# Kernel optimization log

Measured on AMD Instinct MI355X. Metric: run time of the kernel, lower is better.

The kernel has to match this reference:

```python
import jax, jax.numpy as jnp
import numpy as np

B, D, H, DOUT, E, K = 8192, 1024, 4096, 1024, 8, 2


def setup_inputs() -> dict:
    key = jax.random.key(0)
    ks = jax.random.split(key, 7)
    s_d = 1.0 / np.sqrt(D)
    s_h = 1.0 / np.sqrt(H)
    return {
        "x": jax.random.normal(ks[0], (B, D), jnp.float32),
        "Wg": jax.random.uniform(ks[1], (D, E), jnp.float32, -s_d, s_d),
        "bg": jax.random.uniform(ks[2], (E,), jnp.float32, -s_d, s_d),
        "W1": jax.random.uniform(ks[3], (E, D, H), jnp.float32, -s_d, s_d),
        "b1": jax.random.uniform(ks[4], (E, H), jnp.float32, -s_d, s_d),
        "W2": jax.random.uniform(ks[5], (E, H, DOUT), jnp.float32, -s_h, s_h),
        "b2": jax.random.uniform(ks[6], (E, DOUT), jnp.float32, -s_h, s_h),
    }


def reference(x, Wg, bg, W1, b1, W2, b2):
    # gating
    gate_probs = jax.nn.softmax(x @ Wg + bg, axis=-1)          # [B, E]
    top_k_probs, top_k_idx = jax.lax.top_k(gate_probs, K)       # [B, K]
    top_k_probs = top_k_probs / jnp.sum(top_k_probs, axis=-1, keepdims=True)

    # dense all-expert compute (faithful to torch.stack over experts)
    h = jax.nn.gelu(jnp.einsum('bd,edh->beh', x, W1) + b1, approximate=False)  # [B, E, H]
    expert_outputs = jnp.einsum('beh,eho->beo', h, W2) + b2                    # [B, E, DOUT]

    # gather selected experts and combine
    sel = jnp.take_along_axis(expert_outputs, top_k_idx[:, :, None], axis=1)   # [B, K, DOUT]
    output = jnp.sum(sel * top_k_probs[:, :, None], axis=1)                    # [B, DOUT]

    # load-balancing aux loss (as written in the original)
    expert_usage = jnp.mean(gate_probs, axis=0)                # [E]
    uniform = jnp.full_like(expert_usage, 1.0 / E)
    aux_loss = jnp.sum(expert_usage * jnp.log(uniform) - jnp.log(expert_usage) * uniform)
    return output, aux_loss
```

## Files before the change

kernel.cpp:

```cpp
#include <hip/hip_runtime.h>
#include <hip/hip_bf16.h>
#include <hip/hip_fp16.h>

#define B_    8192
#define D_    1024
#define H_    4096
#define DOUT_ 1024
#define E_    8
#define MAXR  17408

typedef float    f32x4 __attribute__((ext_vector_type(4)));
typedef _Float16 f16x8 __attribute__((ext_vector_type(8)));
typedef unsigned short u16;
typedef u16      u16x8 __attribute__((ext_vector_type(8)));
typedef u16      u16x4 __attribute__((ext_vector_type(4)));
typedef unsigned int u32;

__device__ __forceinline__ u16 f2h_bits(float f) {
  _Float16 h = (_Float16)f;
  return __builtin_bit_cast(u16, h);
}
__device__ __forceinline__ float h2f(u16 b) {
  return (float)__builtin_bit_cast(_Float16, b);
}

__device__ __forceinline__ float gelu_f(float v) {
  float z = 0.7978845608028654f * (v + 0.044715f * v * v * v);
  float ez = __expf(2.f * z);
  float th = 1.f - 2.f / (ez + 1.f);
  return 0.5f * v * (1.f + th);
}

#define OFF_TOPI 512
#define OFF_TOPW (OFF_TOPI + 65536)
#define OFF_ATOK (OFF_TOPW + 65536)
#define OFF_WSL  (OFF_ATOK + 69632)
#define OFF_SLOT (OFF_WSL + 69632)
#define OFF_XG   524288
#define OFF_W1T  (OFF_XG + 35651584)
#define OFF_W2T  OFF_XG
#define OFF_Y    (OFF_XG + 67108864)
#define OFF_HB   (OFF_W1T + 67108864)

__global__ void k_init(int* __restrict__ atok, float* __restrict__ wslot,
                       int* __restrict__ meta) {
  int i = blockIdx.x * 256 + threadIdx.x;
  if (i < MAXR) { atok[i] = 0; wslot[i] = 0.f; }
  if (blockIdx.x == 0 && threadIdx.x < 64) meta[threadIdx.x] = 0;
}

__global__ __launch_bounds__(256) void k_gate(
    const float* __restrict__ x, const float* __restrict__ Wg,
    const float* __restrict__ bg, int* __restrict__ counts,
    float* __restrict__ usage, int* __restrict__ topi, float* __restrict__ topw) {
  __shared__ float su[E_];
  if (threadIdx.x < E_) su[threadIdx.x] = 0.f;
  __syncthreads();
  const int lane = threadIdx.x & 63;
  const int b = blockIdx.x * 4 + (threadIdx.x >> 6);
  float p[E_] = {0.f,0.f,0.f,0.f,0.f,0.f,0.f,0.f};
  #pragma unroll
  for (int j = 0; j < 4; ++j) {
    int d = j * 256 + lane * 4;
    float4 xv = *(const float4*)&x[(size_t)b * D_ + d];
    const float* wr = &Wg[(size_t)d * E_];
    #pragma unroll
    for (int c = 0; c < 4; ++c) {
      float xc = reinterpret_cast<const float*>(&xv)[c];
      #pragma unroll
      for (int e = 0; e < E_; ++e) p[e] += xc * wr[c * E_ + e];
    }
  }
  #pragma unroll
  for (int off = 32; off >= 1; off >>= 1)
    #pragma unroll
    for (int e = 0; e < E_; ++e) p[e] += __shfl_xor(p[e], off, 64);
  float mx = -1e30f;
  #pragma unroll
  for (int e = 0; e < E_; ++e) { p[e] += bg[e]; mx = fmaxf(mx, p[e]); }
  int i0 = 0; float l0 = p[0];
  #pragma unroll
  for (int e = 1; e < E_; ++e) if (p[e] > l0) { l0 = p[e]; i0 = e; }
  int i1 = -1; float l1 = -1e30f;
  #pragma unroll
  for (int e = 0; e < E_; ++e) if (e != i0 && p[e] > l1) { l1 = p[e]; i1 = e; }
  float s = 0.f;
  #pragma unroll
  for (int e = 0; e < E_; ++e) { p[e] = expf(p[e] - mx); s += p[e]; }
  float inv = 1.f / s;
  if (lane == 0) {
    float e0 = expf(l0 - mx), e1 = expf(l1 - mx);
    float wsum = e0 + e1;
    topi[b * 2] = i0; topi[b * 2 + 1] = i1;
    topw[b * 2] = e0 / wsum; topw[b * 2 + 1] = e1 / wsum;
    atomicAdd(&counts[i0], 1);
    atomicAdd(&counts[i1], 1);
    #pragma unroll
    for (int e = 0; e < E_; ++e) atomicAdd(&su[e], p[e] * inv);
  }
  __syncthreads();
  if (threadIdx.x < E_) atomicAdd(&usage[threadIdx.x], su[threadIdx.x]);
}

__global__ void k_scan_aux(const int* __restrict__ counts, int* __restrict__ offsets,
                           const float* __restrict__ usage, float* __restrict__ auxp) {
  if (threadIdx.x == 0) {
    int off = 0;
    for (int e = 0; e < E_; ++e) { offsets[e] = off; off += (counts[e] + 127) & ~127; }
    offsets[E_] = off;
    float aux = 0.f;
    const float lu = logf(1.0f / (float)E_);
    for (int e = 0; e < E_; ++e) {
      float u = usage[e] * (1.0f / (float)B_);
      aux += u * lu - logf(u) * (1.0f / (float)E_);
    }
    *auxp = aux;
  }
}

__global__ void k_scatter(const int* __restrict__ topi, const float* __restrict__ topw,
                          const int* __restrict__ offsets, int* __restrict__ cursors,
                          int* __restrict__ atok, float* __restrict__ wslot,
                          int* __restrict__ slot_of) {
  int b = blockIdx.x * 256 + threadIdx.x;
  if (b >= B_) return;
  #pragma unroll
  for (int k = 0; k < 2; ++k) {
    int e = topi[b * 2 + k];
    int pos = atomicAdd(&cursors[e], 1);
    int slot = offsets[e] + pos;
    atok[slot] = b;
    wslot[slot] = topw[b * 2 + k];
    slot_of[b * 2 + k] = slot;
  }
}

__global__ __launch_bounds__(256) void k_gather(const float* __restrict__ x,
                                                const int* __restrict__ atok,
                                                u16* __restrict__ Xg) {
  int slot = blockIdx.x;
  int tok = atok[slot];
  int c = threadIdx.x * 4;
  float4 v = *(const float4*)&x[(size_t)tok * D_ + c];
  const float* vf = reinterpret_cast<const float*>(&v);
  u16x4 o;
  o.x = f2h_bits(vf[0]); o.y = f2h_bits(vf[1]);
  o.z = f2h_bits(vf[2]); o.w = f2h_bits(vf[3]);
  *(u16x4*)&Xg[(size_t)slot * D_ + c] = o;
}

__global__ __launch_bounds__(256) void k_cvt_t(const float* __restrict__ src,
                                               u16* __restrict__ dst, int K, int N) {
  const int e = blockIdx.z;
  const int kt = blockIdx.x * 64;
  const int nt = blockIdx.y * 64;
  __shared__ u16 t[64][68];
  const float* s = src + (size_t)e * K * N;
  u16* d = dst + (size_t)e * N * K;
  const int tr = threadIdx.x >> 4;
  const int tc = threadIdx.x & 15;
  #pragma unroll
  for (int i = 0; i < 4; ++i) {
    int k = tr + i * 16;
    float4 v = *(const float4*)&s[(size_t)(kt + k) * N + nt + tc * 4];
    t[k][tc*4+0] = f2h_bits(v.x); t[k][tc*4+1] = f2h_bits(v.y);
    t[k][tc*4+2] = f2h_bits(v.z); t[k][tc*4+3] = f2h_bits(v.w);
  }
  __syncthreads();
  #pragma unroll
  for (int i = 0; i < 4; ++i) {
    int n = tr + i * 16;
    u16x4 o;
    o.x = t[tc*4+0][n]; o.y = t[tc*4+1][n];
    o.z = t[tc*4+2][n]; o.w = t[tc*4+3][n];
    *(u16x4*)&d[(size_t)(nt + n) * K + kt + tc * 4] = o;
  }
}

#define GLDS(g, l) __builtin_amdgcn_global_load_lds( \
    (const u32 __attribute__((address_space(1)))*)(g), \
    (u32 __attribute__((address_space(3)))*)(l), 16, 0, 0)

#define VMWAIT(N) asm volatile("s_waitcnt vmcnt(" #N ")" ::: "memory")
#define BARRIER() do { __builtin_amdgcn_s_barrier(); \
                       asm volatile("" ::: "memory"); } while (0)

#define NXT(x) ((x) == 24576 ? 0 : (x) + 12288)

#define STG3(LDK, kt, sb) do { \
  const int r_ = lane >> 2; \
  const int sc_ = ((lane & 3) ^ ((r_ ^ (r_ >> 2)) & 3)) * 8; \
  { \
    int rw = wid * 16 + r_; \
    GLDS(Ap + (size_t)rw * (LDK) + (kt) * 32 + sc_, SM + (sb) + wid * 512); \
  } \
  _Pragma("unroll") \
  for (int j = 0; j < 2; ++j) { \
    int seg = wid * 2 + j; \
    GLDS(Bp + (size_t)(seg * 16 + r_) * (LDK) + (kt) * 32 + sc_, \
         SM + (sb) + 4096 + seg * 512); \
  } } while (0)

#define RD_FR(rb_) do { \
  const int r15_ = lane & 15; \
  const int co_ = (((lane >> 4) ^ ((r15_ ^ (r15_ >> 2)) & 3)) * 8); \
  _Pragma("unroll") \
  for (int mi = 0; mi < 4; ++mi) \
    af[mi] = *(const f16x8*)&SM[(rb_) + (wr * 64 + mi * 16 + r15_) * 32 + co_]; \
  _Pragma("unroll") \
  for (int n = 0; n < 4; ++n) \
    bf[n] = *(const f16x8*)&SM[(rb_) + 4096 + (wc * 64 + n * 16 + r15_) * 32 + co_]; \
} while (0)

#define MM16() do { \
  __builtin_amdgcn_s_setprio(1); \
  _Pragma("unroll") \
  for (int mi = 0; mi < 4; ++mi) \
    _Pragma("unroll") \
    for (int n = 0; n < 4; ++n) \
      acc[mi][n] = __builtin_amdgcn_mfma_f32_16x16x32_f16(af[mi], bf[n], acc[mi][n], 0, 0, 0); \
  __builtin_amdgcn_s_setprio(0); \
} while (0)

#define KLOOP(LDK, NT) do { \
  int rb = 0, wb = 24576; \
  STG3(LDK, 0, 0); \
  STG3(LDK, 1, 12288); \
  VMWAIT(3); \
  BARRIER(); \
  for (int t = 0; t < (NT); ++t) { \
    RD_FR(rb); \
    if (t + 2 < (NT)) STG3(LDK, t + 2, wb); \
    BARRIER(); \
    MM16(); \
    if (t + 2 < (NT)) VMWAIT(3); \
    else if (t + 1 < (NT)) VMWAIT(0); \
    BARRIER(); \
    rb = NXT(rb); wb = NXT(wb); \
  } \
} while (0)

__global__ __launch_bounds__(512, 4) void k_gemm1(
    const u16* __restrict__ Xg, const u16* __restrict__ W1t,
    const float* __restrict__ b1, const int* __restrict__ offsets,
    u16* __restrict__ Hb) {
  const int L = blockIdx.x;
  const int mtile = L >> 4;
  const int nt = L & 15;
  const int row0 = mtile * 128;
  if (row0 >= offsets[E_]) return;
  int e = 0;
  #pragma unroll
  for (int i = 1; i < E_; ++i) e = (row0 >= offsets[i]) ? i : e;
  const int n0 = nt * 256;
  const int tid = threadIdx.x, lane = tid & 63, wid = tid >> 6;
  const int wr = wid >> 2, wc = wid & 3;
  __shared__ __align__(16) u16 SM[36864];
  f32x4 acc[4][4] = {};
  f16x8 af[4], bf[4];
  const u16* Ap = Xg + (size_t)row0 * D_;
  const u16* Bp = W1t + (size_t)e * H_ * D_ + (size_t)n0 * D_;

  KLOOP(D_, 32);

  const int rhi = (lane >> 4) * 4, cix = lane & 15;
  float bv[4];
  #pragma unroll
  for (int n = 0; n < 4; ++n) bv[n] = b1[e * H_ + n0 + wc * 64 + n * 16 + cix];
  #pragma unroll
  for (int r = 0; r < 2; ++r) {
    if (wr == r) {
      #pragma unroll
      for (int m = 0; m < 4; ++m)
        #pragma unroll
        for (int n = 0; n < 4; ++n)
          #pragma unroll
          for (int j = 0; j < 4; ++j)
            SM[(m * 16 + rhi + j) * 264 + wc * 64 + n * 16 + cix] =
                f2h_bits(gelu_f(acc[m][n][j] + bv[n]));
    }
    __syncthreads();
    {
      const int rl = tid >> 3, co = (tid & 7) * 32;
      u16* dst = &Hb[(size_t)(row0 + r * 64 + rl) * H_ + n0 + co];
      const u16* srcp = &SM[rl * 264 + co];
      #pragma unroll
      for (int qq = 0; qq < 4; ++qq)
        *(u16x8*)(dst + qq * 8) = *(const u16x8*)(srcp + qq * 8);
    }
    __syncthreads();
  }
}

__global__ __launch_bounds__(512, 4) void k_gemm2(
    const u16* __restrict__ Hb, const u16* __restrict__ W2t,
    const float* __restrict__ b2, const int* __restrict__ offsets,
    u16* __restrict__ Y) {
  const int L = blockIdx.x;
  const int mtile = L >> 2;
  const int nt = L & 3;
  const int row0 = mtile * 128;
  if (row0 >= offsets[E_]) return;
  int e = 0;
  #pragma unroll
  for (int i = 1; i < E_; ++i) e = (row0 >= offsets[i]) ? i : e;
  const int n0 = nt * 256;
  const int tid = threadIdx.x, lane = tid & 63, wid = tid >> 6;
  const int wr = wid >> 2, wc = wid & 3;
  __shared__ __align__(16) u16 SM[36864];
  f32x4 acc[4][4] = {};
  f16x8 af[4], bf[4];
  const u16* Ap = Hb + (size_t)row0 * H_;
  const u16* Bp = W2t + (size_t)e * DOUT_ * H_ + (size_t)n0 * H_;

  KLOOP(H_, 128);

  const int rhi = (lane >> 4) * 4, cix = lane & 15;
  float bv[4];
  #pragma unroll
  for (int n = 0; n < 4; ++n) bv[n] = b2[e * DOUT_ + n0 + wc * 64 + n * 16 + cix];
  #pragma unroll
  for (int r = 0; r < 2; ++r) {
    if (wr == r) {
      #pragma unroll
      for (int m = 0; m < 4; ++m)
        #pragma unroll
        for (int n = 0; n < 4; ++n)
          #pragma unroll
          for (int j = 0; j < 4; ++j)
            SM[(m * 16 + rhi + j) * 264 + wc * 64 + n * 16 + cix] =
                f2h_bits(acc[m][n][j] + bv[n]);
    }
    __syncthreads();
    {
      const int rl = tid >> 3, co = (tid & 7) * 32;
      u16* dst = &Y[(size_t)(row0 + r * 64 + rl) * DOUT_ + n0 + co];
      const u16* srcp = &SM[rl * 264 + co];
      #pragma unroll
      for (int qq = 0; qq < 4; ++qq)
        *(u16x8*)(dst + qq * 8) = *(const u16x8*)(srcp + qq * 8);
    }
    __syncthreads();
  }
}

__global__ __launch_bounds__(256) void k_combine(
    const u16* __restrict__ Y, const float* __restrict__ topw,
    const int* __restrict__ slot_of, float* __restrict__ out) {
  const int b = blockIdx.x;
  const int c = threadIdx.x * 4;
  const int s0 = slot_of[b * 2], s1 = slot_of[b * 2 + 1];
  const float w0 = topw[b * 2], w1 = topw[b * 2 + 1];
  u16x4 y0 = *(const u16x4*)&Y[(size_t)s0 * DOUT_ + c];
  u16x4 y1 = *(const u16x4*)&Y[(size_t)s1 * DOUT_ + c];
  float4 o;
  o.x = w0 * h2f(y0.x) + w1 * h2f(y1.x);
  o.y = w0 * h2f(y0.y) + w1 * h2f(y1.y);
  o.z = w0 * h2f(y0.z) + w1 * h2f(y1.z);
  o.w = w0 * h2f(y0.w) + w1 * h2f(y1.w);
  *(float4*)&out[(size_t)b * DOUT_ + c] = o;
}

extern "C" void kernel_launch(void* const* d_in, const int* in_sizes, int n_in,
                              void* d_out, int out_size, void* d_ws, size_t ws_size,
                              hipStream_t stream) {
  const float* x  = (const float*)d_in[0];
  const float* Wg = (const float*)d_in[1];
  const float* bg = (const float*)d_in[2];
  const float* W1 = (const float*)d_in[3];
  const float* b1 = (const float*)d_in[4];
  const float* W2 = (const float*)d_in[5];
  const float* b2 = (const float*)d_in[6];
  float* out = (float*)d_out;

  char* ws = (char*)d_ws;
  int*   counts  = (int*)(ws + 0);
  int*   cursors = (int*)(ws + 32);
  int*   offsets = (int*)(ws + 64);
  float* usage   = (float*)(ws + 128);
  int*   topi    = (int*)(ws + OFF_TOPI);
  float* topw    = (float*)(ws + OFF_TOPW);
  int*   atok    = (int*)(ws + OFF_ATOK);
  float* wslot   = (float*)(ws + OFF_WSL);
  int*   slot_of = (int*)(ws + OFF_SLOT);
  u16*   Xg      = (u16*)(ws + OFF_XG);
  u16*   W1t     = (u16*)(ws + OFF_W1T);
  u16*   W2t     = (u16*)(ws + OFF_W2T);
  u16*   Y       = (u16*)(ws + OFF_Y);
  u16*   Hb      = (u16*)(ws + OFF_HB);

  k_init<<<(MAXR + 255) / 256, 256, 0, stream>>>(atok, wslot, (int*)ws);
  k_gate<<<B_ / 4, 256, 0, stream>>>(x, Wg, bg, counts, usage, topi, topw);
  k_scan_aux<<<1, 64, 0, stream>>>(counts, offsets, usage, out + (size_t)B_ * DOUT_);
  k_scatter<<<B_ / 256, 256, 0, stream>>>(topi, topw, offsets, cursors, atok, wslot, slot_of);
  k_gather<<<MAXR, 256, 0, stream>>>(x, atok, Xg);
  k_cvt_t<<<dim3(D_ / 64, H_ / 64, E_), 256, 0, stream>>>(W1, W1t, D_, H_);
  k_gemm1<<<(MAXR / 128) * 16, 512, 0, stream>>>(Xg, W1t, b1, offsets, Hb);
  k_cvt_t<<<dim3(H_ / 64, DOUT_ / 64, E_), 256, 0, stream>>>(W2, W2t, H_, DOUT_);
  k_gemm2<<<(MAXR / 128) * 4, 512, 0, stream>>>(Hb, W2t, b2, offsets, Y);
  k_combine<<<B_, 256, 0, stream>>>(Y, topw, slot_of, out);
}
```

Baseline: 800.6 us.

## Remap GEMM tiles per XCD, widen transpose stores, drop unused slot weights

```diff
diff --git a/kernel.cpp b/kernel.cpp
--- a/kernel.cpp
+++ b/kernel.cpp
@@ -34,18 +34,16 @@
 #define OFF_TOPI 512
 #define OFF_TOPW (OFF_TOPI + 65536)
 #define OFF_ATOK (OFF_TOPW + 65536)
-#define OFF_WSL  (OFF_ATOK + 69632)
-#define OFF_SLOT (OFF_WSL + 69632)
+#define OFF_SLOT (OFF_ATOK + 69632)
 #define OFF_XG   524288
 #define OFF_W1T  (OFF_XG + 35651584)
 #define OFF_W2T  OFF_XG
 #define OFF_Y    (OFF_XG + 67108864)
 #define OFF_HB   (OFF_W1T + 67108864)
 
-__global__ void k_init(int* __restrict__ atok, float* __restrict__ wslot,
-                       int* __restrict__ meta) {
+__global__ void k_init(int* __restrict__ atok, int* __restrict__ meta) {
   int i = blockIdx.x * 256 + threadIdx.x;
-  if (i < MAXR) { atok[i] = 0; wslot[i] = 0.f; }
+  if (i < MAXR) atok[i] = 0;
   if (blockIdx.x == 0 && threadIdx.x < 64) meta[threadIdx.x] = 0;
 }
 
@@ -118,9 +116,8 @@
   }
 }
 
-__global__ void k_scatter(const int* __restrict__ topi, const float* __restrict__ topw,
-                          const int* __restrict__ offsets, int* __restrict__ cursors,
-                          int* __restrict__ atok, float* __restrict__ wslot,
+__global__ void k_scatter(const int* __restrict__ topi, const int* __restrict__ offsets,
+                          int* __restrict__ cursors, int* __restrict__ atok,
                           int* __restrict__ slot_of) {
   int b = blockIdx.x * 256 + threadIdx.x;
   if (b >= B_) return;
@@ -130,7 +127,6 @@
     int pos = atomicAdd(&cursors[e], 1);
     int slot = offsets[e] + pos;
     atok[slot] = b;
-    wslot[slot] = topw[b * 2 + k];
     slot_of[b * 2 + k] = slot;
   }
 }
@@ -154,27 +150,26 @@
   const int e = blockIdx.z;
   const int kt = blockIdx.x * 64;
   const int nt = blockIdx.y * 64;
-  __shared__ u16 t[64][68];
+  __shared__ __align__(16) u16 t[64][72];
   const float* s = src + (size_t)e * K * N;
   u16* d = dst + (size_t)e * N * K;
-  const int tr = threadIdx.x >> 4;
-  const int tc = threadIdx.x & 15;
+  const int nq = threadIdx.x & 15;
+  const int kr = threadIdx.x >> 4;
   #pragma unroll
   for (int i = 0; i < 4; ++i) {
-    int k = tr + i * 16;
-    float4 v = *(const float4*)&s[(size_t)(kt + k) * N + nt + tc * 4];
-    t[k][tc*4+0] = f2h_bits(v.x); t[k][tc*4+1] = f2h_bits(v.y);
-    t[k][tc*4+2] = f2h_bits(v.z); t[k][tc*4+3] = f2h_bits(v.w);
+    int k = kr + i * 16;
+    float4 v = *(const float4*)&s[(size_t)(kt + k) * N + nt + nq * 4];
+    t[nq*4+0][k] = f2h_bits(v.x); t[nq*4+1][k] = f2h_bits(v.y);
+    t[nq*4+2][k] = f2h_bits(v.z); t[nq*4+3][k] = f2h_bits(v.w);
   }
   __syncthreads();
-  #pragma unroll
-  for (int i = 0; i < 4; ++i) {
-    int n = tr + i * 16;
-    u16x4 o;
-    o.x = t[tc*4+0][n]; o.y = t[tc*4+1][n];
-    o.z = t[tc*4+2][n]; o.w = t[tc*4+3][n];
-    *(u16x4*)&d[(size_t)(nt + n) * K + kt + tc * 4] = o;
-  }
+  const int n = threadIdx.x >> 2;
+  const int kq = threadIdx.x & 3;
+  u16x8 a = *(const u16x8*)&t[n][kq * 16];
+  u16x8 b = *(const u16x8*)&t[n][kq * 16 + 8];
+  u16* dp = &d[(size_t)(nt + n) * K + kt + kq * 16];
+  *(u16x8*)(dp) = a;
+  *(u16x8*)(dp + 8) = b;
 }
 
 #define GLDS(g, l) __builtin_amdgcn_global_load_lds( \
@@ -245,8 +240,10 @@
     const float* __restrict__ b1, const int* __restrict__ offsets,
     u16* __restrict__ Hb) {
   const int L = blockIdx.x;
-  const int mtile = L >> 4;
-  const int nt = L & 15;
+  const int xcd = L & 7;
+  const int s = L >> 3;
+  const int nt = s & 15;
+  const int mtile = ((s >> 4) << 3) | xcd;
   const int row0 = mtile * 128;
   if (row0 >= offsets[E_]) return;
   int e = 0;
@@ -297,8 +294,10 @@
     const float* __restrict__ b2, const int* __restrict__ offsets,
     u16* __restrict__ Y) {
   const int L = blockIdx.x;
-  const int mtile = L >> 2;
-  const int nt = L & 3;
+  const int xcd = L & 7;
+  const int s = L >> 3;
+  const int nt = s & 3;
+  const int mtile = ((s >> 2) << 3) | xcd;
   const int row0 = mtile * 128;
   if (row0 >= offsets[E_]) return;
   int e = 0;
@@ -381,7 +380,6 @@
   int*   topi    = (int*)(ws + OFF_TOPI);
   float* topw    = (float*)(ws + OFF_TOPW);
   int*   atok    = (int*)(ws + OFF_ATOK);
-  float* wslot   = (float*)(ws + OFF_WSL);
   int*   slot_of = (int*)(ws + OFF_SLOT);
   u16*   Xg      = (u16*)(ws + OFF_XG);
   u16*   W1t     = (u16*)(ws + OFF_W1T);
@@ -389,10 +387,10 @@
   u16*   Y       = (u16*)(ws + OFF_Y);
   u16*   Hb      = (u16*)(ws + OFF_HB);
 
-  k_init<<<(MAXR + 255) / 256, 256, 0, stream>>>(atok, wslot, (int*)ws);
+  k_init<<<(MAXR + 255) / 256, 256, 0, stream>>>(atok, (int*)ws);
   k_gate<<<B_ / 4, 256, 0, stream>>>(x, Wg, bg, counts, usage, topi, topw);
   k_scan_aux<<<1, 64, 0, stream>>>(counts, offsets, usage, out + (size_t)B_ * DOUT_);
-  k_scatter<<<B_ / 256, 256, 0, stream>>>(topi, topw, offsets, cursors, atok, wslot, slot_of);
+  k_scatter<<<B_ / 256, 256, 0, stream>>>(topi, offsets, cursors, atok, slot_of);
   k_gather<<<MAXR, 256, 0, stream>>>(x, atok, Xg);
   k_cvt_t<<<dim3(D_ / 64, H_ / 64, E_), 256, 0, stream>>>(W1, W1t, D_, H_);
   k_gemm1<<<(MAXR / 128) * 16, 512, 0, stream>>>(Xg, W1t, b1, offsets, Hb);
```

Result: slower. 817.2 us (+2.1%).
